# Kernel optimization log

Measured on AMD Instinct MI355X. Metric: run time of the kernel, lower is better.

Reference implementation:

```python
import jax, jax.numpy as jnp
import numpy as np
import math

NUM_BLOCKS = 8
SPARSITY_THRESHOLD = 0.01
HARD_FRAC = 1.0
HIDDEN_SIZE = 1024
HIDDEN_FACTOR = 2
SCALE = 0.02


def _dht1d(x, axis):
    # Discrete Hartley transform along `axis`: sum x * cas(2*pi*k*n/N)
    # cas = cos + sin, equivalently Re(FFT) - Im(FFT).
    F = jnp.fft.fft(x, axis=axis)
    return F.real - F.imag


def dht2d(x):
    # Separable 2D Hartley transform over the spatial axes (1, 2) of (B,H,W,C).
    return _dht1d(_dht1d(x, 1), 2)


def setup_inputs() -> dict:
    key = jax.random.key(0)
    k_x, k_w1, k_b1, k_w2, k_b2 = jax.random.split(key, 5)
    B, N, C = 4, 16384, HIDDEN_SIZE
    bs = C // NUM_BLOCKS                      # 128
    hid = bs * HIDDEN_FACTOR                  # 256
    x = jax.random.normal(k_x, (B, N, C), dtype=jnp.float32)
    w1 = SCALE * jax.random.normal(k_w1, (2, NUM_BLOCKS, bs, hid), dtype=jnp.float32)
    b1 = SCALE * jax.random.normal(k_b1, (2, NUM_BLOCKS, hid), dtype=jnp.float32)
    w2 = SCALE * jax.random.normal(k_w2, (2, NUM_BLOCKS, hid, bs), dtype=jnp.float32)
    b2 = SCALE * jax.random.normal(k_b2, (2, NUM_BLOCKS, bs), dtype=jnp.float32)
    return {"x": x, "w1": w1, "b1": b1, "w2": w2, "b2": b2}


def reference(x, w1, b1, w2, b2):
    bias = x
    B, N, C = x.shape
    H = W = int(math.sqrt(N))
    bs = C // NUM_BLOCKS

    xs = x.reshape(B, H, W, C)
    xs = dht2d(xs)                                    # spatial Hartley domain
    xs = xs.reshape(B, H, W, NUM_BLOCKS, bs)

    kept = int(math.sqrt(H * W) * HARD_FRAC)          # = H when frac == 1
    xk = xs[:, :kept, :kept]                          # (B, kept, kept, nb, bs)

    # Block-diagonal spectral MLP; the source sums contributions from both
    # weight slices w[0] and w[1] with bias b[0].
    o1 = jax.nn.relu(
        jnp.einsum("bxyni,nio->bxyno", xk, w1[0])
        + jnp.einsum("bxyni,nio->bxyno", xk, w1[1])
        + b1[0]
    )                                                 # (B, kept, kept, nb, hid)
    o2k = (
        jnp.einsum("bxyno,noi->bxyni", o1, w2[0])
        + jnp.einsum("bxyno,noi->bxyni", o1, w2[1])
        + b2[0]
    )                                                 # (B, kept, kept, nb, bs)

    o2 = jnp.zeros_like(xs).at[:, :kept, :kept].set(o2k)

    # softshrink
    lam = jnp.float32(SPARSITY_THRESHOLD)
    z = jnp.sign(o2) * jax.nn.relu(jnp.abs(o2) - lam)

    z = z.reshape(B, H, W, C)
    z = dht2d(z) / (H * W)                            # inverse Hartley
    return z.reshape(B, N, C) + bias
```

## Files before the change

kernel.cpp:

```cpp
#include <hip/hip_runtime.h>

typedef unsigned short u16;
typedef unsigned int   u32;
typedef __attribute__((ext_vector_type(8))) short bf16x8;
typedef __attribute__((ext_vector_type(4))) short bf16x4;
typedef __attribute__((ext_vector_type(4))) float f32x4;

#define LAM 0.01f

__device__ __forceinline__ u16 f2bf(float f){
  u32 u = __float_as_uint(f);
  u = u + 0x7FFFu + ((u >> 16) & 1u);
  return (u16)(u >> 16);
}

__device__ __forceinline__ int swz(int row, int k){
  return row*128 + ((((k >> 3) ^ row) & 15) << 3) + (k & 7);
}

#define MFMA16(ac, a, b) ac = __builtin_amdgcn_mfma_f32_16x16x32_bf16((a), (b), (ac), 0, 0, 0)

#define GEMM_STEP(acc, A0,A1,A2,A3, B0,B1,B2,B3) \
  MFMA16(acc[0], A0,B0); MFMA16(acc[1], A0,B1); MFMA16(acc[2], A0,B2); MFMA16(acc[3], A0,B3); \
  MFMA16(acc[4], A1,B0); MFMA16(acc[5], A1,B1); MFMA16(acc[6], A1,B2); MFMA16(acc[7], A1,B3); \
  MFMA16(acc[8], A2,B0); MFMA16(acc[9], A2,B1); MFMA16(acc[10],A2,B2); MFMA16(acc[11],A2,B3); \
  MFMA16(acc[12],A3,B0); MFMA16(acc[13],A3,B1); MFMA16(acc[14],A3,B2); MFMA16(acc[15],A3,B3);

__global__ void k_prep(const float* __restrict__ w1, const float* __restrict__ w2,
                       u16* __restrict__ Mg, u16* __restrict__ W1et, u16* __restrict__ W2et){
  int gid = blockIdx.x * 256 + threadIdx.x;
  if (gid < 16384){
    int i = gid >> 7, j = gid & 127;
    int t = (i * j) & 127;
    float ang = (float)t * 0.04908738521234052f;
    Mg[gid] = f2bf(cosf(ang) + sinf(ang));
  } else if (gid < 16384 + 262144){
    int e = gid - 16384;
    int n = e >> 15, o = (e >> 7) & 255, i = e & 127;
    float v = w1[(n*128 + i)*256 + o] + w1[((8+n)*128 + i)*256 + o];
    W1et[e] = f2bf(v);
  } else {
    int e = gid - (16384 + 262144);
    int n = e >> 15, i = (e >> 8) & 127, o = e & 255;
    float v = w2[(n*256 + o)*128 + i] + w2[((8+n)*256 + o)*128 + i];
    W2et[e] = f2bf(v);
  }
}

__launch_bounds__(256, 2)
__global__ void k_dht_fwd(const float* __restrict__ x, const u16* __restrict__ Mg,
                          u16* __restrict__ Ag){
  __shared__ u16 xt[128*128];
  __shared__ u16 st[128*128];
  int bi = blockIdx.x;
  int n = bi & 7, w = (bi >> 3) & 127, b = bi >> 10;
  int tid = threadIdx.x;
  int lane = tid & 63, wid = tid >> 6;
  int l15 = lane & 15, q = lane >> 4;
  int r0 = (wid >> 1) * 64, c0 = (wid & 1) * 64;

  {
    int c = tid & 127, hg = tid >> 7;
    const float* xb = x + ((b*128)*128 + w)*1024 + n*128 + c;
    for (int it = 0; it < 32; ++it){
      int h0 = (hg + 2*it) * 2;
      float v0 = xb[h0 * 131072];
      float v1 = xb[(h0+1) * 131072];
      u32 pk = (u32)f2bf(v0) | ((u32)f2bf(v1) << 16);
      *(u32*)(&xt[swz(c, h0)]) = pk;
    }
  }
  __syncthreads();

  f32x4 acc[16];
#pragma unroll
  for (int t = 0; t < 16; ++t) acc[t] = f32x4{0.f,0.f,0.f,0.f};

#pragma unroll
  for (int ks = 0; ks < 4; ++ks){
    int kk = ks*32 + q*8;
    bf16x8 a0 = *(const bf16x8*)(Mg + (r0 +  0 + l15)*128 + kk);
    bf16x8 a1 = *(const bf16x8*)(Mg + (r0 + 16 + l15)*128 + kk);
    bf16x8 a2 = *(const bf16x8*)(Mg + (r0 + 32 + l15)*128 + kk);
    bf16x8 a3 = *(const bf16x8*)(Mg + (r0 + 48 + l15)*128 + kk);
    bf16x8 b0 = *(const bf16x8*)(&xt[swz(c0 +  0 + l15, kk)]);
    bf16x8 b1 = *(const bf16x8*)(&xt[swz(c0 + 16 + l15, kk)]);
    bf16x8 b2 = *(const bf16x8*)(&xt[swz(c0 + 32 + l15, kk)]);
    bf16x8 b3 = *(const bf16x8*)(&xt[swz(c0 + 48 + l15, kk)]);
    GEMM_STEP(acc, a0,a1,a2,a3, b0,b1,b2,b3);
  }

#pragma unroll
  for (int i = 0; i < 4; ++i){
    int rb = r0 + 16*i + q*4;
#pragma unroll
    for (int j = 0; j < 4; ++j){
      int col = c0 + 16*j + l15;
      f32x4 v = acc[i*4+j];
      st[swz(rb+0, col)] = f2bf(v.x);
      st[swz(rb+1, col)] = f2bf(v.y);
      st[swz(rb+2, col)] = f2bf(v.z);
      st[swz(rb+3, col)] = f2bf(v.w);
    }
  }
  __syncthreads();
  u16* Aout = Ag + ((b*128)*128 + w)*1024 + n*128;
#pragma unroll
  for (int it = 0; it < 8; ++it){
    int cid = it*256 + tid;
    int row = cid >> 4, cp = cid & 15;
    bf16x8 v = *(const bf16x8*)(&st[row*128 + (((cp ^ row) & 15) << 3)]);
    *(bf16x8*)(Aout + row*131072 + cp*8) = v;
  }
}

__launch_bounds__(256, 2)
__global__ void k_mlp(const u16* __restrict__ Xg, const u16* __restrict__ W1et,
                      const u16* __restrict__ W2et, const u16* __restrict__ Mg,
                      const float* __restrict__ b1g, const float* __restrict__ b2g,
                      u16* __restrict__ Ug){
  __shared__ u16 bufA[128*128];
  __shared__ u16 bufB[128*128];
  int bi = blockIdx.x;
  int n = bi & 7, h = (bi >> 3) & 127, b = bi >> 10;
  int tid = threadIdx.x;
  int lane = tid & 63, wid = tid >> 6;
  int l15 = lane & 15, q = lane >> 4;
  int r0 = (wid >> 1) * 64, c0 = (wid & 1) * 64;

  const u16*  Xbase  = Xg + ((b*128 + h)*128)*1024 + n*128;
  const u16*  W1base = W1et + n*256*128;
  const u16*  W2base = W2et + n*128*256;
  const float* b1base = b1g + n*256;
  const float* b2base = b2g + n*128;

  f32x4 acc2[16], acc1[16];
#pragma unroll
  for (int t = 0; t < 16; ++t) acc2[t] = f32x4{0.f,0.f,0.f,0.f};

  for (int half = 0; half < 2; ++half){
#pragma unroll
    for (int t = 0; t < 16; ++t) acc1[t] = f32x4{0.f,0.f,0.f,0.f};
#pragma unroll
    for (int ks = 0; ks < 4; ++ks){
      int kk = ks*32 + q*8;
      bf16x8 a0 = *(const bf16x8*)(Xbase + (r0 +  0 + l15)*1024 + kk);
      bf16x8 a1 = *(const bf16x8*)(Xbase + (r0 + 16 + l15)*1024 + kk);
      bf16x8 a2 = *(const bf16x8*)(Xbase + (r0 + 32 + l15)*1024 + kk);
      bf16x8 a3 = *(const bf16x8*)(Xbase + (r0 + 48 + l15)*1024 + kk);
      const u16* wb = W1base + (half*128 + c0 + l15)*128 + kk;
      bf16x8 b0 = *(const bf16x8*)(wb);
      bf16x8 b1 = *(const bf16x8*)(wb + 16*128);
      bf16x8 b2 = *(const bf16x8*)(wb + 32*128);
      bf16x8 b3 = *(const bf16x8*)(wb + 48*128);
      GEMM_STEP(acc1, a0,a1,a2,a3, b0,b1,b2,b3);
    }
#pragma unroll
    for (int i = 0; i < 4; ++i){
      int kw = r0 + 16*i + q*4;
#pragma unroll
      for (int j = 0; j < 4; ++j){
        int row = c0 + 16*j + l15;
        f32x4 v = acc1[i*4+j];
        bf16x4 pk;
        pk.x = (short)f2bf(v.x); pk.y = (short)f2bf(v.y);
        pk.z = (short)f2bf(v.z); pk.w = (short)f2bf(v.w);
        *(bf16x4*)(&bufA[swz(row, kw)]) = pk;
      }
    }
    __syncthreads();

#pragma unroll
    for (int t = 0; t < 16; ++t) acc1[t] = f32x4{0.f,0.f,0.f,0.f};
#pragma unroll
    for (int ks = 0; ks < 4; ++ks){
      int kk = ks*32 + q*8;
      bf16x8 a0 = *(const bf16x8*)(&bufA[swz(r0 +  0 + l15, kk)]);
      bf16x8 a1 = *(const bf16x8*)(&bufA[swz(r0 + 16 + l15, kk)]);
      bf16x8 a2 = *(const bf16x8*)(&bufA[swz(r0 + 32 + l15, kk)]);
      bf16x8 a3 = *(const bf16x8*)(&bufA[swz(r0 + 48 + l15, kk)]);
      bf16x8 b0 = *(const bf16x8*)(Mg + (c0 +  0 + l15)*128 + kk);
      bf16x8 b1 = *(const bf16x8*)(Mg + (c0 + 16 + l15)*128 + kk);
      bf16x8 b2 = *(const bf16x8*)(Mg + (c0 + 32 + l15)*128 + kk);
      bf16x8 b3 = *(const bf16x8*)(Mg + (c0 + 48 + l15)*128 + kk);
      GEMM_STEP(acc1, a0,a1,a2,a3, b0,b1,b2,b3);
    }
#pragma unroll
    for (int i = 0; i < 4; ++i){
      int ko = r0 + 16*i + q*4;
      float bs0 = b1base[half*128 + ko + 0];
      float bs1 = b1base[half*128 + ko + 1];
      float bs2 = b1base[half*128 + ko + 2];
      float bs3 = b1base[half*128 + ko + 3];
#pragma unroll
      for (int j = 0; j < 4; ++j){
        int row = c0 + 16*j + l15;
        f32x4 v = acc1[i*4+j];
        bf16x4 pk;
        pk.x = (short)f2bf(fmaxf(v.x + bs0, 0.f));
        pk.y = (short)f2bf(fmaxf(v.y + bs1, 0.f));
        pk.z = (short)f2bf(fmaxf(v.z + bs2, 0.f));
        pk.w = (short)f2bf(fmaxf(v.w + bs3, 0.f));
        *(bf16x4*)(&bufB[swz(row, ko)]) = pk;
      }
    }
    __syncthreads();

#pragma unroll
    for (int ks = 0; ks < 4; ++ks){
      int kk = ks*32 + q*8;
      bf16x8 a0 = *(const bf16x8*)(&bufB[swz(r0 +  0 + l15, kk)]);
      bf16x8 a1 = *(const bf16x8*)(&bufB[swz(r0 + 16 + l15, kk)]);
      bf16x8 a2 = *(const bf16x8*)(&bufB[swz(r0 + 32 + l15, kk)]);
      bf16x8 a3 = *(const bf16x8*)(&bufB[swz(r0 + 48 + l15, kk)]);
      const u16* wb = W2base + (c0 + l15)*256 + half*128 + kk;
      bf16x8 b0 = *(const bf16x8*)(wb);
      bf16x8 b1 = *(const bf16x8*)(wb + 16*256);
      bf16x8 b2 = *(const bf16x8*)(wb + 32*256);
      bf16x8 b3 = *(const bf16x8*)(wb + 48*256);
      GEMM_STEP(acc2, a0,a1,a2,a3, b0,b1,b2,b3);
    }
    __syncthreads();
  }

  {
    float b2v[4];
#pragma unroll
    for (int j = 0; j < 4; ++j) b2v[j] = b2base[c0 + 16*j + l15];
#pragma unroll
    for (int i = 0; i < 4; ++i){
      int kw = r0 + 16*i + q*4;
#pragma unroll
      for (int j = 0; j < 4; ++j){
        int row = c0 + 16*j + l15;
        f32x4 v = acc2[i*4+j];
        float t0 = v.x + b2v[j], t1 = v.y + b2v[j], t2 = v.z + b2v[j], t3 = v.w + b2v[j];
        float m0 = fmaxf(fabsf(t0) - LAM, 0.f);
        float m1 = fmaxf(fabsf(t1) - LAM, 0.f);
        float m2 = fmaxf(fabsf(t2) - LAM, 0.f);
        float m3 = fmaxf(fabsf(t3) - LAM, 0.f);
        bf16x4 pk;
        pk.x = (short)f2bf(t0 >= 0.f ? m0 : -m0);
        pk.y = (short)f2bf(t1 >= 0.f ? m1 : -m1);
        pk.z = (short)f2bf(t2 >= 0.f ? m2 : -m2);
        pk.w = (short)f2bf(t3 >= 0.f ? m3 : -m3);
        *(bf16x4*)(&bufA[swz(row, kw)]) = pk;
      }
    }
  }
  __syncthreads();

#pragma unroll
  for (int t = 0; t < 16; ++t) acc1[t] = f32x4{0.f,0.f,0.f,0.f};
#pragma unroll
  for (int ks = 0; ks < 4; ++ks){
    int kk = ks*32 + q*8;
    bf16x8 a0 = *(const bf16x8*)(Mg + (r0 +  0 + l15)*128 + kk);
    bf16x8 a1 = *(const bf16x8*)(Mg + (r0 + 16 + l15)*128 + kk);
    bf16x8 a2 = *(const bf16x8*)(Mg + (r0 + 32 + l15)*128 + kk);
    bf16x8 a3 = *(const bf16x8*)(Mg + (r0 + 48 + l15)*128 + kk);
    bf16x8 b0 = *(const bf16x8*)(&bufA[swz(c0 +  0 + l15, kk)]);
    bf16x8 b1 = *(const bf16x8*)(&bufA[swz(c0 + 16 + l15, kk)]);
    bf16x8 b2 = *(const bf16x8*)(&bufA[swz(c0 + 32 + l15, kk)]);
    bf16x8 b3 = *(const bf16x8*)(&bufA[swz(c0 + 48 + l15, kk)]);
    GEMM_STEP(acc1, a0,a1,a2,a3, b0,b1,b2,b3);
  }
#pragma unroll
  for (int i = 0; i < 4; ++i){
    int rb = r0 + 16*i + q*4;
#pragma unroll
    for (int j = 0; j < 4; ++j){
      int col = c0 + 16*j + l15;
      f32x4 v = acc1[i*4+j];
      bufB[swz(rb+0, col)] = f2bf(v.x);
      bufB[swz(rb+1, col)] = f2bf(v.y);
      bufB[swz(rb+2, col)] = f2bf(v.z);
      bufB[swz(rb+3, col)] = f2bf(v.w);
    }
  }
  __syncthreads();
  u16* Ubase = Ug + ((b*128 + h)*128)*1024 + n*128;
#pragma unroll
  for (int it = 0; it < 8; ++it){
    int cid = it*256 + tid;
    int row = cid >> 4, cp = cid & 15;
    bf16x8 v = *(const bf16x8*)(&bufB[row*128 + (((cp ^ row) & 15) << 3)]);
    *(bf16x8*)(Ubase + row*1024 + cp*8) = v;
  }
}

__launch_bounds__(256, 2)
__global__ void k_dht_inv(const u16* __restrict__ Ug, const u16* __restrict__ Mg,
                          const float* __restrict__ x, float* __restrict__ out){
  __shared__ u16 ut[128*128];
  int bi = blockIdx.x;
  int n = bi & 7, w = (bi >> 3) & 127, b = bi >> 10;
  int tid = threadIdx.x;
  int lane = tid & 63, wid = tid >> 6;
  int l15 = lane & 15, q = lane >> 4;
  int r0 = (wid >> 1) * 64, c0 = (wid & 1) * 64;

  {
    int cp = (tid & 63) * 2, hb = (tid >> 6) * 2;
    const u16* Ub = Ug + ((b*128)*128 + w)*1024 + n*128;
#pragma unroll
    for (int it = 0; it < 16; ++it){
      int h0 = hb + it*8;
      u32 d0 = *(const u32*)(Ub + h0*131072 + cp);
      u32 d1 = *(const u32*)(Ub + (h0+1)*131072 + cp);
      u32 lo = (d0 & 0xFFFFu) | ((d1 & 0xFFFFu) << 16);
      u32 hi = (d0 >> 16) | (d1 & 0xFFFF0000u);
      *(u32*)(&ut[swz(cp,   h0)]) = lo;
      *(u32*)(&ut[swz(cp+1, h0)]) = hi;
    }
  }
  __syncthreads();

  f32x4 acc[16];
#pragma unroll
  for (int t = 0; t < 16; ++t) acc[t] = f32x4{0.f,0.f,0.f,0.f};

#pragma unroll
  for (int ks = 0; ks < 4; ++ks){
    int kk = ks*32 + q*8;
    bf16x8 a0 = *(const bf16x8*)(Mg + (r0 +  0 + l15)*128 + kk);
    bf16x8 a1 = *(const bf16x8*)(Mg + (r0 + 16 + l15)*128 + kk);
    bf16x8 a2 = *(const bf16x8*)(Mg + (r0 + 32 + l15)*128 + kk);
    bf16x8 a3 = *(const bf16x8*)(Mg + (r0 + 48 + l15)*128 + kk);
    bf16x8 b0 = *(const bf16x8*)(&ut[swz(c0 +  0 + l15, kk)]);
    bf16x8 b1 = *(const bf16x8*)(&ut[swz(c0 + 16 + l15, kk)]);
    bf16x8 b2 = *(const bf16x8*)(&ut[swz(c0 + 32 + l15, kk)]);
    bf16x8 b3 = *(const bf16x8*)(&ut[swz(c0 + 48 + l15, kk)]);
    GEMM_STEP(acc, a0,a1,a2,a3, b0,b1,b2,b3);
  }

  const float s = 1.f / 16384.f;
  int gbase = ((b*128)*128 + w)*1024 + n*128;
#pragma unroll
  for (int i = 0; i < 4; ++i){
    int hh = r0 + 16*i + q*4;
#pragma unroll
    for (int j = 0; j < 4; ++j){
      int cc = c0 + 16*j + l15;
      f32x4 v = acc[i*4+j];
      int i0 = gbase + (hh+0)*131072 + cc; out[i0] = v.x * s + x[i0];
      int i1 = gbase + (hh+1)*131072 + cc; out[i1] = v.y * s + x[i1];
      int i2 = gbase + (hh+2)*131072 + cc; out[i2] = v.z * s + x[i2];
      int i3 = gbase + (hh+3)*131072 + cc; out[i3] = v.w * s + x[i3];
    }
  }
}

extern "C" void kernel_launch(void* const* d_in, const int* in_sizes, int n_in,
                              void* d_out, int out_size, void* d_ws, size_t ws_size,
                              hipStream_t stream) {
  const float* x  = (const float*)d_in[0];
  const float* w1 = (const float*)d_in[1];
  const float* b1 = (const float*)d_in[2];
  const float* w2 = (const float*)d_in[3];
  const float* b2 = (const float*)d_in[4];
  float* out = (float*)d_out;

  u16* Ag   = (u16*)d_out;
  u16* W1et = (u16*)((char*)d_out + 267386880);
  u16* W2et = (u16*)((char*)d_out + 267911168);
  u16* Ug   = (u16*)d_ws;
  u16* Mg   = (u16*)((char*)d_ws + 134217728);

  k_prep<<<2112, 256, 0, stream>>>(w1, w2, Mg, W1et, W2et);
  k_dht_fwd<<<4096, 256, 0, stream>>>(x, Mg, Ag);
  k_mlp<<<4096, 256, 0, stream>>>(Ag, W1et, W2et, Mg, b1, b2, Ug);
  k_dht_inv<<<4096, 256, 0, stream>>>(Ug, Mg, x, out);
}
```

Baseline: 1.102 ms.

## Raise occupancy: reuse LDS in forward DHT, split MLP across 8 waves

```diff
diff --git a/kernel.cpp b/kernel.cpp
--- a/kernel.cpp
+++ b/kernel.cpp
@@ -25,6 +25,10 @@
   MFMA16(acc[4], A1,B0); MFMA16(acc[5], A1,B1); MFMA16(acc[6], A1,B2); MFMA16(acc[7], A1,B3); \
   MFMA16(acc[8], A2,B0); MFMA16(acc[9], A2,B1); MFMA16(acc[10],A2,B2); MFMA16(acc[11],A2,B3); \
   MFMA16(acc[12],A3,B0); MFMA16(acc[13],A3,B1); MFMA16(acc[14],A3,B2); MFMA16(acc[15],A3,B3);
+
+#define GEMM_STEP8(acc, A0,A1, B0,B1,B2,B3) \
+  MFMA16(acc[0], A0,B0); MFMA16(acc[1], A0,B1); MFMA16(acc[2], A0,B2); MFMA16(acc[3], A0,B3); \
+  MFMA16(acc[4], A1,B0); MFMA16(acc[5], A1,B1); MFMA16(acc[6], A1,B2); MFMA16(acc[7], A1,B3);
 
 __global__ void k_prep(const float* __restrict__ w1, const float* __restrict__ w2,
                        u16* __restrict__ Mg, u16* __restrict__ W1et, u16* __restrict__ W2et){
@@ -47,11 +51,10 @@
   }
 }
 
-__launch_bounds__(256, 2)
+__launch_bounds__(256, 4)
 __global__ void k_dht_fwd(const float* __restrict__ x, const u16* __restrict__ Mg,
                           u16* __restrict__ Ag){
   __shared__ u16 xt[128*128];
-  __shared__ u16 st[128*128];
   int bi = blockIdx.x;
   int n = bi & 7, w = (bi >> 3) & 127, b = bi >> 10;
   int tid = threadIdx.x;
@@ -89,6 +92,7 @@
     bf16x8 b3 = *(const bf16x8*)(&xt[swz(c0 + 48 + l15, kk)]);
     GEMM_STEP(acc, a0,a1,a2,a3, b0,b1,b2,b3);
   }
+  __syncthreads();
 
 #pragma unroll
   for (int i = 0; i < 4; ++i){
@@ -97,10 +101,10 @@
     for (int j = 0; j < 4; ++j){
       int col = c0 + 16*j + l15;
       f32x4 v = acc[i*4+j];
-      st[swz(rb+0, col)] = f2bf(v.x);
-      st[swz(rb+1, col)] = f2bf(v.y);
-      st[swz(rb+2, col)] = f2bf(v.z);
-      st[swz(rb+3, col)] = f2bf(v.w);
+      xt[swz(rb+0, col)] = f2bf(v.x);
+      xt[swz(rb+1, col)] = f2bf(v.y);
+      xt[swz(rb+2, col)] = f2bf(v.z);
+      xt[swz(rb+3, col)] = f2bf(v.w);
     }
   }
   __syncthreads();
@@ -109,12 +113,12 @@
   for (int it = 0; it < 8; ++it){
     int cid = it*256 + tid;
     int row = cid >> 4, cp = cid & 15;
-    bf16x8 v = *(const bf16x8*)(&st[row*128 + (((cp ^ row) & 15) << 3)]);
+    bf16x8 v = *(const bf16x8*)(&xt[row*128 + (((cp ^ row) & 15) << 3)]);
     *(bf16x8*)(Aout + row*131072 + cp*8) = v;
   }
 }
 
-__launch_bounds__(256, 2)
+__launch_bounds__(512, 4)
 __global__ void k_mlp(const u16* __restrict__ Xg, const u16* __restrict__ W1et,
                       const u16* __restrict__ W2et, const u16* __restrict__ Mg,
                       const float* __restrict__ b1g, const float* __restrict__ b2g,
@@ -126,7 +130,7 @@
   int tid = threadIdx.x;
   int lane = tid & 63, wid = tid >> 6;
   int l15 = lane & 15, q = lane >> 4;
-  int r0 = (wid >> 1) * 64, c0 = (wid & 1) * 64;
+  int r0 = (wid >> 1) * 32, c0 = (wid & 1) * 64;
 
   const u16*  Xbase  = Xg + ((b*128 + h)*128)*1024 + n*128;
   const u16*  W1base = W1et + n*256*128;
@@ -134,29 +138,27 @@
   const float* b1base = b1g + n*256;
   const float* b2base = b2g + n*128;
 
-  f32x4 acc2[16], acc1[16];
-#pragma unroll
-  for (int t = 0; t < 16; ++t) acc2[t] = f32x4{0.f,0.f,0.f,0.f};
+  f32x4 acc2[8], acc1[8];
+#pragma unroll
+  for (int t = 0; t < 8; ++t) acc2[t] = f32x4{0.f,0.f,0.f,0.f};
 
   for (int half = 0; half < 2; ++half){
 #pragma unroll
-    for (int t = 0; t < 16; ++t) acc1[t] = f32x4{0.f,0.f,0.f,0.f};
+    for (int t = 0; t < 8; ++t) acc1[t] = f32x4{0.f,0.f,0.f,0.f};
 #pragma unroll
     for (int ks = 0; ks < 4; ++ks){
       int kk = ks*32 + q*8;
       bf16x8 a0 = *(const bf16x8*)(Xbase + (r0 +  0 + l15)*1024 + kk);
       bf16x8 a1 = *(const bf16x8*)(Xbase + (r0 + 16 + l15)*1024 + kk);
-      bf16x8 a2 = *(const bf16x8*)(Xbase + (r0 + 32 + l15)*1024 + kk);
-      bf16x8 a3 = *(const bf16x8*)(Xbase + (r0 + 48 + l15)*1024 + kk);
       const u16* wb = W1base + (half*128 + c0 + l15)*128 + kk;
       bf16x8 b0 = *(const bf16x8*)(wb);
       bf16x8 b1 = *(const bf16x8*)(wb + 16*128);
       bf16x8 b2 = *(const bf16x8*)(wb + 32*128);
       bf16x8 b3 = *(const bf16x8*)(wb + 48*128);
-      GEMM_STEP(acc1, a0,a1,a2,a3, b0,b1,b2,b3);
-    }
-#pragma unroll
-    for (int i = 0; i < 4; ++i){
+      GEMM_STEP8(acc1, a0,a1, b0,b1,b2,b3);
+    }
+#pragma unroll
+    for (int i = 0; i < 2; ++i){
       int kw = r0 + 16*i + q*4;
 #pragma unroll
       for (int j = 0; j < 4; ++j){
@@ -171,22 +173,20 @@
     __syncthreads();
 
 #pragma unroll
-    for (int t = 0; t < 16; ++t) acc1[t] = f32x4{0.f,0.f,0.f,0.f};
+    for (int t = 0; t < 8; ++t) acc1[t] = f32x4{0.f,0.f,0.f,0.f};
 #pragma unroll
     for (int ks = 0; ks < 4; ++ks){
       int kk = ks*32 + q*8;
       bf16x8 a0 = *(const bf16x8*)(&bufA[swz(r0 +  0 + l15, kk)]);
       bf16x8 a1 = *(const bf16x8*)(&bufA[swz(r0 + 16 + l15, kk)]);
-      bf16x8 a2 = *(const bf16x8*)(&bufA[swz(r0 + 32 + l15, kk)]);
-      bf16x8 a3 = *(const bf16x8*)(&bufA[swz(r0 + 48 + l15, kk)]);
       bf16x8 b0 = *(const bf16x8*)(Mg + (c0 +  0 + l15)*128 + kk);
       bf16x8 b1 = *(const bf16x8*)(Mg + (c0 + 16 + l15)*128 + kk);
       bf16x8 b2 = *(const bf16x8*)(Mg + (c0 + 32 + l15)*128 + kk);
       bf16x8 b3 = *(const bf16x8*)(Mg + (c0 + 48 + l15)*128 + kk);
-      GEMM_STEP(acc1, a0,a1,a2,a3, b0,b1,b2,b3);
-    }
-#pragma unroll
-    for (int i = 0; i < 4; ++i){
+      GEMM_STEP8(acc1, a0,a1, b0,b1,b2,b3);
+    }
+#pragma unroll
+    for (int i = 0; i < 2; ++i){
       int ko = r0 + 16*i + q*4;
       float bs0 = b1base[half*128 + ko + 0];
       float bs1 = b1base[half*128 + ko + 1];
@@ -211,14 +211,12 @@
       int kk = ks*32 + q*8;
       bf16x8 a0 = *(const bf16x8*)(&bufB[swz(r0 +  0 + l15, kk)]);
       bf16x8 a1 = *(const bf16x8*)(&bufB[swz(r0 + 16 + l15, kk)]);
-      bf16x8 a2 = *(const bf16x8*)(&bufB[swz(r0 + 32 + l15, kk)]);
-      bf16x8 a3 = *(const bf16x8*)(&bufB[swz(r0 + 48 + l15, kk)]);
       const u16* wb = W2base + (c0 + l15)*256 + half*128 + kk;
       bf16x8 b0 = *(const bf16x8*)(wb);
       bf16x8 b1 = *(const bf16x8*)(wb + 16*256);
       bf16x8 b2 = *(const bf16x8*)(wb + 32*256);
       bf16x8 b3 = *(const bf16x8*)(wb + 48*256);
-      GEMM_STEP(acc2, a0,a1,a2,a3, b0,b1,b2,b3);
+      GEMM_STEP8(acc2, a0,a1, b0,b1,b2,b3);
     }
     __syncthreads();
   }
@@ -228,7 +226,7 @@
 #pragma unroll
     for (int j = 0; j < 4; ++j) b2v[j] = b2base[c0 + 16*j + l15];
 #pragma unroll
-    for (int i = 0; i < 4; ++i){
+    for (int i = 0; i < 2; ++i){
       int kw = r0 + 16*i + q*4;
 #pragma unroll
       for (int j = 0; j < 4; ++j){
@@ -251,22 +249,20 @@
   __syncthreads();
 
 #pragma unroll
-  for (int t = 0; t < 16; ++t) acc1[t] = f32x4{0.f,0.f,0.f,0.f};
+  for (int t = 0; t < 8; ++t) acc1[t] = f32x4{0.f,0.f,0.f,0.f};
 #pragma unroll
   for (int ks = 0; ks < 4; ++ks){
     int kk = ks*32 + q*8;
     bf16x8 a0 = *(const bf16x8*)(Mg + (r0 +  0 + l15)*128 + kk);
     bf16x8 a1 = *(const bf16x8*)(Mg + (r0 + 16 + l15)*128 + kk);
-    bf16x8 a2 = *(const bf16x8*)(Mg + (r0 + 32 + l15)*128 + kk);
-    bf16x8 a3 = *(const bf16x8*)(Mg + (r0 + 48 + l15)*128 + kk);
     bf16x8 b0 = *(const bf16x8*)(&bufA[swz(c0 +  0 + l15, kk)]);
     bf16x8 b1 = *(const bf16x8*)(&bufA[swz(c0 + 16 + l15, kk)]);
     bf16x8 b2 = *(const bf16x8*)(&bufA[swz(c0 + 32 + l15, kk)]);
     bf16x8 b3 = *(const bf16x8*)(&bufA[swz(c0 + 48 + l15, kk)]);
-    GEMM_STEP(acc1, a0,a1,a2,a3, b0,b1,b2,b3);
-  }
-#pragma unroll
-  for (int i = 0; i < 4; ++i){
+    GEMM_STEP8(acc1, a0,a1, b0,b1,b2,b3);
+  }
+#pragma unroll
+  for (int i = 0; i < 2; ++i){
     int rb = r0 + 16*i + q*4;
 #pragma unroll
     for (int j = 0; j < 4; ++j){
@@ -281,15 +277,15 @@
   __syncthreads();
   u16* Ubase = Ug + ((b*128 + h)*128)*1024 + n*128;
 #pragma unroll
-  for (int it = 0; it < 8; ++it){
-    int cid = it*256 + tid;
+  for (int it = 0; it < 4; ++it){
+    int cid = it*512 + tid;
     int row = cid >> 4, cp = cid & 15;
     bf16x8 v = *(const bf16x8*)(&bufB[row*128 + (((cp ^ row) & 15) << 3)]);
     *(bf16x8*)(Ubase + row*1024 + cp*8) = v;
   }
 }
 
-__launch_bounds__(256, 2)
+__launch_bounds__(256, 4)
 __global__ void k_dht_inv(const u16* __restrict__ Ug, const u16* __restrict__ Mg,
                           const float* __restrict__ x, float* __restrict__ out){
   __shared__ u16 ut[128*128];
@@ -369,6 +365,6 @@
 
   k_prep<<<2112, 256, 0, stream>>>(w1, w2, Mg, W1et, W2et);
   k_dht_fwd<<<4096, 256, 0, stream>>>(x, Mg, Ag);
-  k_mlp<<<4096, 256, 0, stream>>>(Ag, W1et, W2et, Mg, b1, b2, Ug);
+  k_mlp<<<4096, 512, 0, stream>>>(Ag, W1et, W2et, Mg, b1, b2, Ug);
   k_dht_inv<<<4096, 256, 0, stream>>>(Ug, Mg, x, out);
 }
```

Result: slower. 1.317 ms (+19.6%).
